# Kernel optimization log

Measured on AMD Instinct MI355X. Metric: run time of the kernel, lower is better.

Reference implementation:

```python
import jax, jax.numpy as jnp
import numpy as np

N, F, H, C, E = 100000, 128, 128, 40, 1600000


def setup_inputs() -> dict:
    key = jax.random.key(0)
    ks = jax.random.split(key, 8)
    x = jax.random.normal(ks[0], (N, F), dtype=jnp.float32)
    edge_index = jax.random.randint(ks[1], (2, E), 0, N, dtype=jnp.int64)
    s = 0.05
    return {
        "x": x,
        "edge_index": edge_index,
        "eps1": jnp.float32(0.0),
        "w1": jax.random.normal(ks[2], (F, H), dtype=jnp.float32) * s,
        "b1": jnp.zeros((H,), jnp.float32),
        "w2": jax.random.normal(ks[3], (H, H), dtype=jnp.float32) * s,
        "b2": jnp.zeros((H,), jnp.float32),
        "eps2": jnp.float32(0.0),
        "w3": jax.random.normal(ks[4], (H, H), dtype=jnp.float32) * s,
        "b3": jnp.zeros((H,), jnp.float32),
        "w4": jax.random.normal(ks[5], (H, C), dtype=jnp.float32) * s,
        "b4": jnp.zeros((C,), jnp.float32),
    }


def _gin_aggregate(h, src, dst, eps, n):
    # sum_{j -> i} h_j  +  (1+eps) * h_i
    agg = jax.ops.segment_sum(h[src], dst, num_segments=n)
    return (1.0 + eps) * h + agg


def reference(x, edge_index, eps1, w1, b1, w2, b2, eps2, w3, b3, w4, b4):
    src, dst = edge_index[0], edge_index[1]
    n = x.shape[0]
    # conv1: GINConv with MLP = Lin-ReLU-Lin-ReLU
    h = _gin_aggregate(x, src, dst, eps1, n)
    h = jax.nn.relu(h @ w1 + b1)
    h = jax.nn.relu(h @ w2 + b2)
    h = jax.nn.relu(h)  # outer F.relu (idempotent, kept for faithfulness)
    # dropout: identity in eval mode
    # conv2: GINConv with MLP = Lin-ReLU-Lin
    h2 = _gin_aggregate(h, src, dst, eps2, n)
    h2 = jax.nn.relu(h2 @ w3 + b3)
    h2 = h2 @ w4 + b4
    return jax.nn.log_softmax(h2, axis=1)
```

## Files before the change

kernel.cpp:

```cpp
#include <hip/hip_runtime.h>
#include <hip/hip_fp16.h>
#include <math.h>

constexpr int F = 128;
constexpr int C = 40;
constexpr int LDH = 136;
constexpr int BSHIFT = 8;
constexpr int BSIZE = 1 << BSHIFT;
constexpr int CHUNK = 8192;

typedef __attribute__((ext_vector_type(8))) _Float16 half8;
typedef __attribute__((ext_vector_type(4))) float float4v;


__global__ __launch_bounds__(256) void coarse_hist_kernel(const int* __restrict__ dst, int E, int NB,
                                                          int* __restrict__ coarse_count) {
    __shared__ int hist[512];
    int t = threadIdx.x;
    int c0 = blockIdx.x * CHUNK;
    int cend = min(c0 + CHUNK, E);
    for (int i = t; i < NB; i += 256) hist[i] = 0;
    __syncthreads();
    for (int i = c0 + t; i < cend; i += 256)
        atomicAdd(&hist[dst[i] >> BSHIFT], 1);
    __syncthreads();
    for (int i = t; i < NB; i += 256)
        if (hist[i]) atomicAdd(&coarse_count[i], hist[i]);
}

__global__ __launch_bounds__(512) void coarse_scan_kernel(const int* __restrict__ coarse_count,
                                                          int NB, int E,
                                                          int* __restrict__ coarse_start,
                                                          int* __restrict__ bucket_pos,
                                                          int* __restrict__ row_start, int N) {
    __shared__ int tmp[512];
    int t = threadIdx.x;
    int v = (t < NB) ? coarse_count[t] : 0;
    tmp[t] = v;
    __syncthreads();
    for (int d = 1; d < 512; d <<= 1) {
        int add = (t >= d) ? tmp[t - d] : 0;
        __syncthreads();
        tmp[t] += add;
        __syncthreads();
    }
    if (t < NB) {
        int ex = tmp[t] - v;
        coarse_start[t] = ex;
        bucket_pos[t] = ex;
    }
    if (t == 0) {
        coarse_start[NB] = E;
        row_start[N] = E;
    }
}

__global__ __launch_bounds__(256) void bucket_scatter_a_kernel(
        const int* __restrict__ src, const int* __restrict__ dst, int E, int NB,
        int* __restrict__ bucket_pos, unsigned* __restrict__ pairs) {
    __shared__ int hist[512];
    __shared__ int base[512];
    int t = threadIdx.x;
    int c0 = blockIdx.x * CHUNK;
    int cend = min(c0 + CHUNK, E);
    for (int i = t; i < NB; i += 256) hist[i] = 0;
    __syncthreads();
    for (int i = c0 + t; i < cend; i += 256)
        atomicAdd(&hist[dst[i] >> BSHIFT], 1);
    __syncthreads();
    for (int i = t; i < NB; i += 256) {
        int h = hist[i];
        base[i] = (h > 0) ? atomicAdd(&bucket_pos[i], h) : 0;
        hist[i] = 0;
    }
    __syncthreads();
    for (int i = c0 + t; i < cend; i += 256) {
        int d = dst[i];
        int b = d >> BSHIFT;
        int p = base[b] + atomicAdd(&hist[b], 1);
        pairs[p] = ((unsigned)(d & (BSIZE - 1)) << 24) | (unsigned)src[i];
    }
}

__global__ __launch_bounds__(256) void bucket_sort_kernel(const unsigned* __restrict__ pairs,
                                                          const int* __restrict__ coarse_start,
                                                          int N, int* __restrict__ row_start,
                                                          int* __restrict__ src_sorted) {
    __shared__ int hist[256];
    __shared__ int tmp[256];
    int b = blockIdx.x, t = threadIdx.x;
    int base = b << BSHIFT;
    int start = coarse_start[b];
    int end = coarse_start[b + 1];
    hist[t] = 0;
    __syncthreads();
    for (int i = start + t; i < end; i += 256)
        atomicAdd(&hist[pairs[i] >> 24], 1);
    __syncthreads();
    int v = hist[t];
    tmp[t] = v;
    __syncthreads();
    for (int d = 1; d < 256; d <<= 1) {
        int add = (t >= d) ? tmp[t - d] : 0;
        __syncthreads();
        tmp[t] += add;
        __syncthreads();
    }
    int ex = start + tmp[t] - v;
    if (base + t < N) row_start[base + t] = ex;
    hist[t] = ex;
    __syncthreads();
    for (int i = start + t; i < end; i += 256) {
        unsigned u = pairs[i];
        int p = atomicAdd(&hist[u >> 24], 1);
        src_sorted[p] = (int)(u & 0x00FFFFFFu);
    }
}


__global__ void conv_f16_kernel(const float* __restrict__ in, __half* __restrict__ out, int n4,
                                int* __restrict__ coarse_count, int NB) {
    int i = blockIdx.x * blockDim.x + threadIdx.x;
    if (blockIdx.x == 0) {
        for (int j = threadIdx.x; j < NB; j += 256) coarse_count[j] = 0;
    }
    if (i >= n4) return;
    float4 v = ((const float4*)in)[i];
    __half2 a = __floats2half2_rn(v.x, v.y);
    __half2 b = __floats2half2_rn(v.z, v.w);
    uint2 o;
    o.x = __builtin_bit_cast(unsigned, a);
    o.y = __builtin_bit_cast(unsigned, b);
    ((uint2*)out)[i] = o;
}


__global__ __launch_bounds__(256) void prep_weights_kernel(
        const float* __restrict__ w1, const float* __restrict__ w2,
        const float* __restrict__ w3, const float* __restrict__ w4,
        __half* __restrict__ w1t, __half* __restrict__ w2t,
        __half* __restrict__ w3t, __half* __restrict__ w4t) {
    __shared__ float lds[128 * 128];
    const float* in; __half* outp; int Nin, Npad;
    switch (blockIdx.x) {
        case 0:  in = w1; outp = w1t; Nin = 128; Npad = 128; break;
        case 1:  in = w2; outp = w2t; Nin = 128; Npad = 128; break;
        case 2:  in = w3; outp = w3t; Nin = 128; Npad = 128; break;
        default: in = w4; outp = w4t; Nin = 40;  Npad = 48;  break;
    }
    int t = threadIdx.x;
    int nf4 = 128 * Nin / 4;
    for (int i = t; i < nf4; i += 256)
        ((float4*)lds)[i] = ((const float4*)in)[i];
    __syncthreads();
    int total = Npad * 64;
    for (int i = t; i < total; i += 256) {
        int n = i >> 6, k2 = (i & 63) * 2;
        float lo = 0.f, hi = 0.f;
        if (n < Nin) {
            lo = lds[k2 * Nin + n];
            hi = lds[(k2 + 1) * Nin + n];
        }
        __half2 h = __floats2half2_rn(lo, hi);
        ((unsigned*)outp)[i] = __builtin_bit_cast(unsigned, h);
    }
}


__global__ __launch_bounds__(256) void agg_f16_kernel(const __half* __restrict__ feat,
        const int* __restrict__ row_start, const int* __restrict__ src_sorted,
        const float* __restrict__ eps_ptr, __half* __restrict__ out, int N) {
    int wid = (int)((blockIdx.x * blockDim.x + threadIdx.x) >> 6);
    int lane = threadIdx.x & 63;
    if (wid >= N) return;
    int q = lane >> 4, l16 = lane & 15;
    int s = row_start[wid], e = row_start[wid + 1];
    uint4 selfu = *(((const uint4*)(feat + (size_t)wid * F)) + l16);
    float ep1 = 1.0f + *eps_ptr;
    __half2 A0, A1, A2, A3, B0, B1, B2, B3;
    A0 = A1 = A2 = A3 = B0 = B1 = B2 = B3 = __builtin_bit_cast(__half2, 0u);
    const uint4 z4 = make_uint4(0u, 0u, 0u, 0u);
    for (int i0 = s; i0 < e; i0 += 16) {
        int li = i0 + l16;
        int sv = src_sorted[li < e ? li : (e - 1)];
        int s0 = __shfl(sv, q);
        int s1 = __shfl(sv, q + 4);
        int s2 = __shfl(sv, q + 8);
        int s3 = __shfl(sv, q + 12);
        uint4 u0 = *(((const uint4*)(feat + (size_t)s0 * F)) + l16);
        uint4 u1 = *(((const uint4*)(feat + (size_t)s1 * F)) + l16);
        uint4 u2 = *(((const uint4*)(feat + (size_t)s2 * F)) + l16);
        uint4 u3 = *(((const uint4*)(feat + (size_t)s3 * F)) + l16);
        if (i0 + q >= e)      u0 = z4;
        if (i0 + q + 4 >= e)  u1 = z4;
        if (i0 + q + 8 >= e)  u2 = z4;
        if (i0 + q + 12 >= e) u3 = z4;
        A0 = __hadd2(A0, __builtin_bit_cast(__half2, u0.x));
        A1 = __hadd2(A1, __builtin_bit_cast(__half2, u0.y));
        A2 = __hadd2(A2, __builtin_bit_cast(__half2, u0.z));
        A3 = __hadd2(A3, __builtin_bit_cast(__half2, u0.w));
        B0 = __hadd2(B0, __builtin_bit_cast(__half2, u1.x));
        B1 = __hadd2(B1, __builtin_bit_cast(__half2, u1.y));
        B2 = __hadd2(B2, __builtin_bit_cast(__half2, u1.z));
        B3 = __hadd2(B3, __builtin_bit_cast(__half2, u1.w));
        A0 = __hadd2(A0, __builtin_bit_cast(__half2, u2.x));
        A1 = __hadd2(A1, __builtin_bit_cast(__half2, u2.y));
        A2 = __hadd2(A2, __builtin_bit_cast(__half2, u2.z));
        A3 = __hadd2(A3, __builtin_bit_cast(__half2, u2.w));
        B0 = __hadd2(B0, __builtin_bit_cast(__half2, u3.x));
        B1 = __hadd2(B1, __builtin_bit_cast(__half2, u3.y));
        B2 = __hadd2(B2, __builtin_bit_cast(__half2, u3.z));
        B3 = __hadd2(B3, __builtin_bit_cast(__half2, u3.w));
    }
    float a[8];
    {
        float2 fa, fb;
        fa = __half22float2(A0); fb = __half22float2(B0); a[0] = fa.x + fb.x; a[1] = fa.y + fb.y;
        fa = __half22float2(A1); fb = __half22float2(B1); a[2] = fa.x + fb.x; a[3] = fa.y + fb.y;
        fa = __half22float2(A2); fb = __half22float2(B2); a[4] = fa.x + fb.x; a[5] = fa.y + fb.y;
        fa = __half22float2(A3); fb = __half22float2(B3); a[6] = fa.x + fb.x; a[7] = fa.y + fb.y;
    }
#pragma unroll
    for (int j = 0; j < 8; ++j) {
        a[j] += __shfl_xor(a[j], 16);
        a[j] += __shfl_xor(a[j], 32);
    }
    if (q == 0) {
        float2 s0 = __half22float2(__builtin_bit_cast(__half2, selfu.x));
        float2 s1 = __half22float2(__builtin_bit_cast(__half2, selfu.y));
        float2 s2 = __half22float2(__builtin_bit_cast(__half2, selfu.z));
        float2 s3 = __half22float2(__builtin_bit_cast(__half2, selfu.w));
        a[0] = fmaf(ep1, s0.x, a[0]); a[1] = fmaf(ep1, s0.y, a[1]);
        a[2] = fmaf(ep1, s1.x, a[2]); a[3] = fmaf(ep1, s1.y, a[3]);
        a[4] = fmaf(ep1, s2.x, a[4]); a[5] = fmaf(ep1, s2.y, a[5]);
        a[6] = fmaf(ep1, s3.x, a[6]); a[7] = fmaf(ep1, s3.y, a[7]);
        uint4 ou;
        ou.x = __builtin_bit_cast(unsigned, __floats2half2_rn(a[0], a[1]));
        ou.y = __builtin_bit_cast(unsigned, __floats2half2_rn(a[2], a[3]));
        ou.z = __builtin_bit_cast(unsigned, __floats2half2_rn(a[4], a[5]));
        ou.w = __builtin_bit_cast(unsigned, __floats2half2_rn(a[6], a[7]));
        *(((uint4*)(out + (size_t)wid * F)) + l16) = ou;
    }
}


__global__ __launch_bounds__(256) void mlp1_mfma_kernel(const __half* __restrict__ A,
        const __half* __restrict__ w1t, const float* __restrict__ b1,
        const __half* __restrict__ w2t, const float* __restrict__ b2,
        __half* __restrict__ out, int N) {
    __shared__ __half ldsA[64 * LDH];
    __shared__ __half ldsW[128 * LDH];
    __shared__ float ldsB[256];
    int t = threadIdx.x;
    int wave = t >> 6, lane = t & 63, quad = lane >> 4, l16 = lane & 15;
    int br = blockIdx.x * 64;
    if (t < 128) ldsB[t] = b1[t];
    else         ldsB[t] = b2[t - 128];
    for (int i = t; i < 1024; i += 256) {
        int r = i >> 4, c = i & 15;
        int gr = br + r;
        uint4 v = make_uint4(0u, 0u, 0u, 0u);
        if (gr < N) v = *((const uint4*)(A + (size_t)gr * F + c * 8));
        *((uint4*)&ldsA[r * LDH + c * 8]) = v;
    }
    for (int i = t; i < 2048; i += 256) {
        int r = i >> 4, c = i & 15;
        *((uint4*)&ldsW[r * LDH + c * 8]) = *((const uint4*)(w1t + r * 128 + c * 8));
    }
    __syncthreads();

    int ct0 = wave * 2;
    float4v acc[4][2];
    float4v zero = {0.f, 0.f, 0.f, 0.f};
#pragma unroll
    for (int i = 0; i < 4; ++i)
#pragma unroll
        for (int j = 0; j < 2; ++j) acc[i][j] = zero;

#pragma unroll
    for (int ks = 0; ks < 4; ++ks) {
        half8 af[4], wf[2];
#pragma unroll
        for (int i = 0; i < 4; ++i)
            af[i] = *((const half8*)&ldsA[(i * 16 + l16) * LDH + ks * 32 + quad * 8]);
#pragma unroll
        for (int j = 0; j < 2; ++j)
            wf[j] = *((const half8*)&ldsW[((ct0 + j) * 16 + l16) * LDH + ks * 32 + quad * 8]);
#pragma unroll
        for (int i = 0; i < 4; ++i)
#pragma unroll
            for (int j = 0; j < 2; ++j)
                acc[i][j] = __builtin_amdgcn_mfma_f32_16x16x32_f16(wf[j], af[i], acc[i][j], 0, 0, 0);
    }
    __syncthreads();
#pragma unroll
    for (int j = 0; j < 2; ++j) {
        int c = ct0 + j;
        float4 bb = *((const float4*)&ldsB[c * 16 + quad * 4]);
#pragma unroll
        for (int i = 0; i < 4; ++i) {
            float v0 = acc[i][j][0] + bb.x; v0 = v0 > 0.f ? v0 : 0.f;
            float v1 = acc[i][j][1] + bb.y; v1 = v1 > 0.f ? v1 : 0.f;
            float v2 = acc[i][j][2] + bb.z; v2 = v2 > 0.f ? v2 : 0.f;
            float v3 = acc[i][j][3] + bb.w; v3 = v3 > 0.f ? v3 : 0.f;
            __half2 h0 = __floats2half2_rn(v0, v1);
            __half2 h1 = __floats2half2_rn(v2, v3);
            uint2 o;
            o.x = __builtin_bit_cast(unsigned, h0);
            o.y = __builtin_bit_cast(unsigned, h1);
            *((uint2*)&ldsA[(i * 16 + l16) * LDH + c * 16 + quad * 4]) = o;
        }
    }
    for (int i = t; i < 2048; i += 256) {
        int r = i >> 4, c = i & 15;
        *((uint4*)&ldsW[r * LDH + c * 8]) = *((const uint4*)(w2t + r * 128 + c * 8));
    }
    __syncthreads();

#pragma unroll
    for (int i = 0; i < 4; ++i)
#pragma unroll
        for (int j = 0; j < 2; ++j) acc[i][j] = zero;
#pragma unroll
    for (int ks = 0; ks < 4; ++ks) {
        half8 af[4], wf[2];
#pragma unroll
        for (int i = 0; i < 4; ++i)
            af[i] = *((const half8*)&ldsA[(i * 16 + l16) * LDH + ks * 32 + quad * 8]);
#pragma unroll
        for (int j = 0; j < 2; ++j)
            wf[j] = *((const half8*)&ldsW[((ct0 + j) * 16 + l16) * LDH + ks * 32 + quad * 8]);
#pragma unroll
        for (int i = 0; i < 4; ++i)
#pragma unroll
            for (int j = 0; j < 2; ++j)
                acc[i][j] = __builtin_amdgcn_mfma_f32_16x16x32_f16(wf[j], af[i], acc[i][j], 0, 0, 0);
    }
    __syncthreads();
#pragma unroll
    for (int j = 0; j < 2; ++j) {
        int c = ct0 + j;
        float4 bb = *((const float4*)&ldsB[128 + c * 16 + quad * 4]);
#pragma unroll
        for (int i = 0; i < 4; ++i) {
            float v0 = acc[i][j][0] + bb.x; v0 = v0 > 0.f ? v0 : 0.f;
            float v1 = acc[i][j][1] + bb.y; v1 = v1 > 0.f ? v1 : 0.f;
            float v2 = acc[i][j][2] + bb.z; v2 = v2 > 0.f ? v2 : 0.f;
            float v3 = acc[i][j][3] + bb.w; v3 = v3 > 0.f ? v3 : 0.f;
            __half2 h0 = __floats2half2_rn(v0, v1);
            __half2 h1 = __floats2half2_rn(v2, v3);
            uint2 o;
            o.x = __builtin_bit_cast(unsigned, h0);
            o.y = __builtin_bit_cast(unsigned, h1);
            *((uint2*)&ldsA[(i * 16 + l16) * LDH + c * 16 + quad * 4]) = o;
        }
    }
    __syncthreads();
    for (int i = t; i < 1024; i += 256) {
        int r = i >> 4, c = i & 15;
        int gr = br + r;
        if (gr < N)
            *((uint4*)(out + (size_t)gr * F + c * 8)) = *((const uint4*)&ldsA[r * LDH + c * 8]);
    }
}


__global__ __launch_bounds__(256) void mlp2_mfma_kernel(const __half* __restrict__ A,
        const __half* __restrict__ w3t, const float* __restrict__ b3,
        const __half* __restrict__ w4t, const float* __restrict__ b4,
        float* __restrict__ out, int N) {
    __shared__ __half ldsA[64 * LDH];
    __shared__ __half ldsW[128 * LDH];
    __shared__ float ldsB[176];
    int t = threadIdx.x;
    int wave = t >> 6, lane = t & 63, quad = lane >> 4, l16 = lane & 15;
    int br = blockIdx.x * 64;
    if (t < 128) ldsB[t] = b3[t];
    else if (t < 176) ldsB[t] = (t - 128 < C) ? b4[t - 128] : 0.f;
    for (int i = t; i < 1024; i += 256) {
        int r = i >> 4, c = i & 15;
        int gr = br + r;
        uint4 v = make_uint4(0u, 0u, 0u, 0u);
        if (gr < N) v = *((const uint4*)(A + (size_t)gr * F + c * 8));
        *((uint4*)&ldsA[r * LDH + c * 8]) = v;
    }
    for (int i = t; i < 2048; i += 256) {
        int r = i >> 4, c = i & 15;
        *((uint4*)&ldsW[r * LDH + c * 8]) = *((const uint4*)(w3t + r * 128 + c * 8));
    }
    __syncthreads();

    int ct0 = wave * 2;
    float4v acc[4][2];
    float4v zero = {0.f, 0.f, 0.f, 0.f};
#pragma unroll
    for (int i = 0; i < 4; ++i)
#pragma unroll
        for (int j = 0; j < 2; ++j) acc[i][j] = zero;
#pragma unroll
    for (int ks = 0; ks < 4; ++ks) {
        half8 af[4], wf[2];
#pragma unroll
        for (int i = 0; i < 4; ++i)
            af[i] = *((const half8*)&ldsA[(i * 16 + l16) * LDH + ks * 32 + quad * 8]);
#pragma unroll
        for (int j = 0; j < 2; ++j)
            wf[j] = *((const half8*)&ldsW[((ct0 + j) * 16 + l16) * LDH + ks * 32 + quad * 8]);
#pragma unroll
        for (int i = 0; i < 4; ++i)
#pragma unroll
            for (int j = 0; j < 2; ++j)
                acc[i][j] = __builtin_amdgcn_mfma_f32_16x16x32_f16(wf[j], af[i], acc[i][j], 0, 0, 0);
    }
    __syncthreads();
#pragma unroll
    for (int j = 0; j < 2; ++j) {
        int c = ct0 + j;
        float4 bb = *((const float4*)&ldsB[c * 16 + quad * 4]);
#pragma unroll
        for (int i = 0; i < 4; ++i) {
            float v0 = acc[i][j][0] + bb.x; v0 = v0 > 0.f ? v0 : 0.f;
            float v1 = acc[i][j][1] + bb.y; v1 = v1 > 0.f ? v1 : 0.f;
            float v2 = acc[i][j][2] + bb.z; v2 = v2 > 0.f ? v2 : 0.f;
            float v3 = acc[i][j][3] + bb.w; v3 = v3 > 0.f ? v3 : 0.f;
            __half2 h0 = __floats2half2_rn(v0, v1);
            __half2 h1 = __floats2half2_rn(v2, v3);
            uint2 o;
            o.x = __builtin_bit_cast(unsigned, h0);
            o.y = __builtin_bit_cast(unsigned, h1);
            *((uint2*)&ldsA[(i * 16 + l16) * LDH + c * 16 + quad * 4]) = o;
        }
    }
    for (int i = t; i < 768; i += 256) {
        int r = i >> 4, c = i & 15;
        *((uint4*)&ldsW[r * LDH + c * 8]) = *((const uint4*)(w4t + r * 128 + c * 8));
    }
    __syncthreads();

    float4v acc4[3];
#pragma unroll
    for (int c = 0; c < 3; ++c) acc4[c] = zero;
#pragma unroll
    for (int ks = 0; ks < 4; ++ks) {
        half8 af = *((const half8*)&ldsA[(wave * 16 + l16) * LDH + ks * 32 + quad * 8]);
#pragma unroll
        for (int c = 0; c < 3; ++c) {
            half8 wf = *((const half8*)&ldsW[(c * 16 + l16) * LDH + ks * 32 + quad * 8]);
            acc4[c] = __builtin_amdgcn_mfma_f32_16x16x32_f16(wf, af, acc4[c], 0, 0, 0);
        }
    }
    float lv[3][4];
#pragma unroll
    for (int c = 0; c < 3; ++c) {
        float4 bb = *((const float4*)&ldsB[128 + c * 16 + quad * 4]);
        lv[c][0] = acc4[c][0] + bb.x;
        lv[c][1] = acc4[c][1] + bb.y;
        lv[c][2] = acc4[c][2] + bb.z;
        lv[c][3] = acc4[c][3] + bb.w;
    }
    bool tile2ok = (quad < 2);
    float m = -1e30f;
#pragma unroll
    for (int c = 0; c < 3; ++c) {
        if (c == 2 && !tile2ok) continue;
#pragma unroll
        for (int r = 0; r < 4; ++r) m = fmaxf(m, lv[c][r]);
    }
    m = fmaxf(m, __shfl_xor(m, 16));
    m = fmaxf(m, __shfl_xor(m, 32));
    float ssum = 0.f;
#pragma unroll
    for (int c = 0; c < 3; ++c) {
        if (c == 2 && !tile2ok) continue;
#pragma unroll
        for (int r = 0; r < 4; ++r) ssum += __expf(lv[c][r] - m);
    }
    ssum += __shfl_xor(ssum, 16);
    ssum += __shfl_xor(ssum, 32);
    float L = m + __logf(ssum);
    int node = br + wave * 16 + l16;
    if (node < N) {
#pragma unroll
        for (int c = 0; c < 3; ++c) {
            if (c == 2 && !tile2ok) continue;
            float4 o = make_float4(lv[c][0] - L, lv[c][1] - L, lv[c][2] - L, lv[c][3] - L);
            *((float4*)(out + (size_t)node * C + c * 16 + quad * 4)) = o;
        }
    }
}


extern "C" void kernel_launch(void* const* d_in, const int* in_sizes, int n_in,
                              void* d_out, int out_size, void* d_ws, size_t ws_size,
                              hipStream_t stream) {
    const float* x    = (const float*)d_in[0];
    const int*   ei   = (const int*)d_in[1];
    const float* eps1 = (const float*)d_in[2];
    const float* w1   = (const float*)d_in[3];
    const float* b1   = (const float*)d_in[4];
    const float* w2   = (const float*)d_in[5];
    const float* b2   = (const float*)d_in[6];
    const float* eps2 = (const float*)d_in[7];
    const float* w3   = (const float*)d_in[8];
    const float* b3   = (const float*)d_in[9];
    const float* w4   = (const float*)d_in[10];
    const float* b4   = (const float*)d_in[11];
    float* out = (float*)d_out;

    int N = in_sizes[0] / F;
    int E = in_sizes[1] / 2;
    const int* src = ei;
    const int* dst = ei + E;

    int NB = (N + BSIZE - 1) >> BSHIFT;
    int BA = (E + CHUNK - 1) / CHUNK;

    __half* x_h  = (__half*)d_ws;
    __half* h0_h = x_h + (size_t)N * F;
    __half* h_h  = h0_h + (size_t)N * F;
    __half* w1t  = h_h + (size_t)N * F;
    __half* w2t  = w1t + 128 * 128;
    __half* w3t  = w2t + 128 * 128;
    __half* w4t  = w3t + 128 * 128;
    unsigned* pairs   = (unsigned*)(w4t + 48 * 128);
    int* row_start    = (int*)(pairs + E);
    int* src_sorted   = row_start + (N + 1);
    int* coarse_count = src_sorted + E;
    int* coarse_start = coarse_count + 512;
    int* bucket_pos   = coarse_start + 513;

    int n4 = N * F / 4;
    conv_f16_kernel<<<(n4 + 255) / 256, 256, 0, stream>>>(x, x_h, n4, coarse_count, NB);
    prep_weights_kernel<<<4, 256, 0, stream>>>(w1, w2, w3, w4, w1t, w2t, w3t, w4t);

    coarse_hist_kernel<<<BA, 256, 0, stream>>>(dst, E, NB, coarse_count);
    coarse_scan_kernel<<<1, 512, 0, stream>>>(coarse_count, NB, E, coarse_start, bucket_pos,
                                              row_start, N);
    bucket_scatter_a_kernel<<<BA, 256, 0, stream>>>(src, dst, E, NB, bucket_pos, pairs);
    bucket_sort_kernel<<<NB, 256, 0, stream>>>(pairs, coarse_start, N, row_start, src_sorted);

    agg_f16_kernel<<<(N + 3) / 4, 256, 0, stream>>>(x_h, row_start, src_sorted, eps1, h0_h, N);
    mlp1_mfma_kernel<<<(N + 63) / 64, 256, 0, stream>>>(h0_h, w1t, b1, w2t, b2, h_h, N);
    agg_f16_kernel<<<(N + 3) / 4, 256, 0, stream>>>(h_h, row_start, src_sorted, eps2, h0_h, N);
    mlp2_mfma_kernel<<<(N + 63) / 64, 256, 0, stream>>>(h0_h, w3t, b3, w4t, b4, out, N);
}
```

Baseline: 346.0 us.

## Replace two-level bucket sort with per-node atomic histogram CSR build and fused prep

```diff
diff --git a/kernel.cpp b/kernel.cpp
--- a/kernel.cpp
+++ b/kernel.cpp
@@ -5,33 +5,86 @@
 constexpr int F = 128;
 constexpr int C = 40;
 constexpr int LDH = 136;
-constexpr int BSHIFT = 8;
-constexpr int BSIZE = 1 << BSHIFT;
-constexpr int CHUNK = 8192;
+constexpr int HCHUNK = 2048;
 
 typedef __attribute__((ext_vector_type(8))) _Float16 half8;
 typedef __attribute__((ext_vector_type(4))) float float4v;
 
 
-__global__ __launch_bounds__(256) void coarse_hist_kernel(const int* __restrict__ dst, int E, int NB,
-                                                          int* __restrict__ coarse_count) {
-    __shared__ int hist[512];
-    int t = threadIdx.x;
-    int c0 = blockIdx.x * CHUNK;
-    int cend = min(c0 + CHUNK, E);
-    for (int i = t; i < NB; i += 256) hist[i] = 0;
-    __syncthreads();
-    for (int i = c0 + t; i < cend; i += 256)
-        atomicAdd(&hist[dst[i] >> BSHIFT], 1);
-    __syncthreads();
-    for (int i = t; i < NB; i += 256)
-        if (hist[i]) atomicAdd(&coarse_count[i], hist[i]);
+__global__ __launch_bounds__(256) void fused_prep_kernel(
+        const float* __restrict__ x, __half* __restrict__ x_h, int n4,
+        const int* __restrict__ dst, int E, int* __restrict__ row_count,
+        const float* __restrict__ w1, const float* __restrict__ w2,
+        const float* __restrict__ w3, const float* __restrict__ w4,
+        __half* __restrict__ w1t, __half* __restrict__ w2t,
+        __half* __restrict__ w3t, __half* __restrict__ w4t, int BH) {
+    __shared__ float smem[4096];
+    int b = blockIdx.x, t = threadIdx.x;
+    if (b < BH) {
+        int c0 = b * HCHUNK, cend = min(c0 + HCHUNK, E);
+        for (int i = c0 + t; i < cend; i += 256)
+            atomicAdd(&row_count[dst[i]], 1);
+        return;
+    }
+    if (b < BH + 4) {
+        const float* in; __half* outp; int Nin, Npad;
+        switch (b - BH) {
+            case 0:  in = w1; outp = w1t; Nin = 128; Npad = 128; break;
+            case 1:  in = w2; outp = w2t; Nin = 128; Npad = 128; break;
+            case 2:  in = w3; outp = w3t; Nin = 128; Npad = 128; break;
+            default: in = w4; outp = w4t; Nin = 40;  Npad = 48;  break;
+        }
+        for (int p = 0; p < 4; ++p) {
+            int nf4 = 32 * Nin / 4;
+            const float4* srcv = (const float4*)(in + 32 * p * Nin);
+            for (int i = t; i < nf4; i += 256) ((float4*)smem)[i] = srcv[i];
+            __syncthreads();
+            int total = Npad * 16;
+            for (int i = t; i < total; i += 256) {
+                int n = i >> 4, wl = i & 15;
+                float lo = 0.f, hi = 0.f;
+                if (n < Nin) {
+                    lo = smem[(2 * wl) * Nin + n];
+                    hi = smem[(2 * wl + 1) * Nin + n];
+                }
+                __half2 h = __floats2half2_rn(lo, hi);
+                ((unsigned*)outp)[n * 64 + 16 * p + wl] = __builtin_bit_cast(unsigned, h);
+            }
+            __syncthreads();
+        }
+        return;
+    }
+    int i = (b - BH - 4) * 256 + t;
+    if (i >= n4) return;
+    float4 v = ((const float4*)x)[i];
+    uint2 o;
+    o.x = __builtin_bit_cast(unsigned, __floats2half2_rn(v.x, v.y));
+    o.y = __builtin_bit_cast(unsigned, __floats2half2_rn(v.z, v.w));
+    ((uint2*)x_h)[i] = o;
+}
+
+
+__global__ __launch_bounds__(256) void node_scan_kernel(int* __restrict__ row_count, int N,
+                                                        int* __restrict__ coarse_count) {
+    __shared__ int tmp[256];
+    int b = blockIdx.x, t = threadIdx.x;
+    int n = (b << 8) + t;
+    int v = (n < N) ? row_count[n] : 0;
+    tmp[t] = v;
+    __syncthreads();
+    for (int d = 1; d < 256; d <<= 1) {
+        int add = (t >= d) ? tmp[t - d] : 0;
+        __syncthreads();
+        tmp[t] += add;
+        __syncthreads();
+    }
+    if (n < N) row_count[n] = tmp[t] - v;
+    if (t == 255) coarse_count[b] = tmp[255];
 }
 
 __global__ __launch_bounds__(512) void coarse_scan_kernel(const int* __restrict__ coarse_count,
                                                           int NB, int E,
                                                           int* __restrict__ coarse_start,
-                                                          int* __restrict__ bucket_pos,
                                                           int* __restrict__ row_start, int N) {
     __shared__ int tmp[512];
     int t = threadIdx.x;
@@ -44,125 +97,33 @@
         tmp[t] += add;
         __syncthreads();
     }
-    if (t < NB) {
-        int ex = tmp[t] - v;
-        coarse_start[t] = ex;
-        bucket_pos[t] = ex;
-    }
+    if (t < NB) coarse_start[t] = tmp[t] - v;
     if (t == 0) {
         coarse_start[NB] = E;
         row_start[N] = E;
     }
 }
 
-__global__ __launch_bounds__(256) void bucket_scatter_a_kernel(
-        const int* __restrict__ src, const int* __restrict__ dst, int E, int NB,
-        int* __restrict__ bucket_pos, unsigned* __restrict__ pairs) {
-    __shared__ int hist[512];
-    __shared__ int base[512];
-    int t = threadIdx.x;
-    int c0 = blockIdx.x * CHUNK;
-    int cend = min(c0 + CHUNK, E);
-    for (int i = t; i < NB; i += 256) hist[i] = 0;
-    __syncthreads();
-    for (int i = c0 + t; i < cend; i += 256)
-        atomicAdd(&hist[dst[i] >> BSHIFT], 1);
-    __syncthreads();
-    for (int i = t; i < NB; i += 256) {
-        int h = hist[i];
-        base[i] = (h > 0) ? atomicAdd(&bucket_pos[i], h) : 0;
-        hist[i] = 0;
-    }
-    __syncthreads();
-    for (int i = c0 + t; i < cend; i += 256) {
-        int d = dst[i];
-        int b = d >> BSHIFT;
-        int p = base[b] + atomicAdd(&hist[b], 1);
-        pairs[p] = ((unsigned)(d & (BSIZE - 1)) << 24) | (unsigned)src[i];
-    }
-}
-
-__global__ __launch_bounds__(256) void bucket_sort_kernel(const unsigned* __restrict__ pairs,
-                                                          const int* __restrict__ coarse_start,
-                                                          int N, int* __restrict__ row_start,
-                                                          int* __restrict__ src_sorted) {
-    __shared__ int hist[256];
-    __shared__ int tmp[256];
-    int b = blockIdx.x, t = threadIdx.x;
-    int base = b << BSHIFT;
-    int start = coarse_start[b];
-    int end = coarse_start[b + 1];
-    hist[t] = 0;
-    __syncthreads();
-    for (int i = start + t; i < end; i += 256)
-        atomicAdd(&hist[pairs[i] >> 24], 1);
-    __syncthreads();
-    int v = hist[t];
-    tmp[t] = v;
-    __syncthreads();
-    for (int d = 1; d < 256; d <<= 1) {
-        int add = (t >= d) ? tmp[t - d] : 0;
-        __syncthreads();
-        tmp[t] += add;
-        __syncthreads();
-    }
-    int ex = start + tmp[t] - v;
-    if (base + t < N) row_start[base + t] = ex;
-    hist[t] = ex;
-    __syncthreads();
-    for (int i = start + t; i < end; i += 256) {
-        unsigned u = pairs[i];
-        int p = atomicAdd(&hist[u >> 24], 1);
-        src_sorted[p] = (int)(u & 0x00FFFFFFu);
-    }
-}
-
-
-__global__ void conv_f16_kernel(const float* __restrict__ in, __half* __restrict__ out, int n4,
-                                int* __restrict__ coarse_count, int NB) {
-    int i = blockIdx.x * blockDim.x + threadIdx.x;
-    if (blockIdx.x == 0) {
-        for (int j = threadIdx.x; j < NB; j += 256) coarse_count[j] = 0;
-    }
-    if (i >= n4) return;
-    float4 v = ((const float4*)in)[i];
-    __half2 a = __floats2half2_rn(v.x, v.y);
-    __half2 b = __floats2half2_rn(v.z, v.w);
-    uint2 o;
-    o.x = __builtin_bit_cast(unsigned, a);
-    o.y = __builtin_bit_cast(unsigned, b);
-    ((uint2*)out)[i] = o;
-}
-
-
-__global__ __launch_bounds__(256) void prep_weights_kernel(
-        const float* __restrict__ w1, const float* __restrict__ w2,
-        const float* __restrict__ w3, const float* __restrict__ w4,
-        __half* __restrict__ w1t, __half* __restrict__ w2t,
-        __half* __restrict__ w3t, __half* __restrict__ w4t) {
-    __shared__ float lds[128 * 128];
-    const float* in; __half* outp; int Nin, Npad;
-    switch (blockIdx.x) {
-        case 0:  in = w1; outp = w1t; Nin = 128; Npad = 128; break;
-        case 1:  in = w2; outp = w2t; Nin = 128; Npad = 128; break;
-        case 2:  in = w3; outp = w3t; Nin = 128; Npad = 128; break;
-        default: in = w4; outp = w4t; Nin = 40;  Npad = 48;  break;
-    }
-    int t = threadIdx.x;
-    int nf4 = 128 * Nin / 4;
-    for (int i = t; i < nf4; i += 256)
-        ((float4*)lds)[i] = ((const float4*)in)[i];
-    __syncthreads();
-    int total = Npad * 64;
-    for (int i = t; i < total; i += 256) {
-        int n = i >> 6, k2 = (i & 63) * 2;
-        float lo = 0.f, hi = 0.f;
-        if (n < Nin) {
-            lo = lds[k2 * Nin + n];
-            hi = lds[(k2 + 1) * Nin + n];
-        }
-        __half2 h = __floats2half2_rn(lo, hi);
-        ((unsigned*)outp)[i] = __builtin_bit_cast(unsigned, h);
+__global__ __launch_bounds__(256) void apply_offsets_kernel(const int* __restrict__ row_count,
+                                                            const int* __restrict__ coarse_start,
+                                                            int N, int* __restrict__ row_start,
+                                                            int* __restrict__ pos) {
+    int n = blockIdx.x * 256 + threadIdx.x;
+    if (n < N) {
+        int rs = row_count[n] + coarse_start[n >> 8];
+        row_start[n] = rs;
+        pos[n] = rs;
+    }
+}
+
+__global__ __launch_bounds__(256) void scatter_kernel(const int* __restrict__ src,
+                                                      const int* __restrict__ dst, int E,
+                                                      int* __restrict__ pos,
+                                                      int* __restrict__ src_sorted) {
+    int c0 = blockIdx.x * HCHUNK, cend = min(c0 + HCHUNK, E);
+    for (int i = c0 + threadIdx.x; i < cend; i += 256) {
+        int p = atomicAdd(&pos[dst[i]], 1);
+        src_sorted[p] = src[i];
     }
 }
 
@@ -512,8 +473,8 @@
     const int* src = ei;
     const int* dst = ei + E;
 
-    int NB = (N + BSIZE - 1) >> BSHIFT;
-    int BA = (E + CHUNK - 1) / CHUNK;
+    int NB = (N + 255) >> 8;
+    int BH = (E + HCHUNK - 1) / HCHUNK;
 
     __half* x_h  = (__half*)d_ws;
     __half* h0_h = x_h + (size_t)N * F;
@@ -522,22 +483,24 @@
     __half* w2t  = w1t + 128 * 128;
     __half* w3t  = w2t + 128 * 128;
     __half* w4t  = w3t + 128 * 128;
-    unsigned* pairs   = (unsigned*)(w4t + 48 * 128);
-    int* row_start    = (int*)(pairs + E);
+    int* row_start    = (int*)(w4t + 48 * 128);
     int* src_sorted   = row_start + (N + 1);
-    int* coarse_count = src_sorted + E;
+    int* row_count    = src_sorted + E;
+    int* pos          = row_count + N;
+    int* coarse_count = pos + N;
     int* coarse_start = coarse_count + 512;
-    int* bucket_pos   = coarse_start + 513;
 
     int n4 = N * F / 4;
-    conv_f16_kernel<<<(n4 + 255) / 256, 256, 0, stream>>>(x, x_h, n4, coarse_count, NB);
-    prep_weights_kernel<<<4, 256, 0, stream>>>(w1, w2, w3, w4, w1t, w2t, w3t, w4t);
-
-    coarse_hist_kernel<<<BA, 256, 0, stream>>>(dst, E, NB, coarse_count);
-    coarse_scan_kernel<<<1, 512, 0, stream>>>(coarse_count, NB, E, coarse_start, bucket_pos,
-                                              row_start, N);
-    bucket_scatter_a_kernel<<<BA, 256, 0, stream>>>(src, dst, E, NB, bucket_pos, pairs);
-    bucket_sort_kernel<<<NB, 256, 0, stream>>>(pairs, coarse_start, N, row_start, src_sorted);
+    int NCONV = (n4 + 255) / 256;
+
+    hipMemsetAsync(row_count, 0, (size_t)N * sizeof(int), stream);
+    fused_prep_kernel<<<BH + 4 + NCONV, 256, 0, stream>>>(x, x_h, n4, dst, E, row_count,
+                                                          w1, w2, w3, w4, w1t, w2t, w3t, w4t, BH);
+
+    node_scan_kernel<<<NB, 256, 0, stream>>>(row_count, N, coarse_count);
+    coarse_scan_kernel<<<1, 512, 0, stream>>>(coarse_count, NB, E, coarse_start, row_start, N);
+    apply_offsets_kernel<<<NB, 256, 0, stream>>>(row_count, coarse_start, N, row_start, pos);
+    scatter_kernel<<<BH, 256, 0, stream>>>(src, dst, E, pos, src_sorted);
 
     agg_f16_kernel<<<(N + 3) / 4, 256, 0, stream>>>(x_h, row_start, src_sorted, eps1, h0_h, N);
     mlp1_mfma_kernel<<<(N + 63) / 64, 256, 0, stream>>>(h0_h, w1t, b1, w2t, b2, h_h, N);
```

After: 476.6 us. 37.7% more time.
